# Performance work log

Measured on AMD Instinct MI355X. Metric: run time of the kernel, lower is better.

Reference implementation:

```python
import jax, jax.numpy as jnp
import numpy as np

B, N, C, H = 4, 4096, 1024, 16
D = C // H


def setup_inputs() -> dict:
    key = jax.random.key(0)
    ks = jax.random.split(key, 15)
    s = 0.02
    f = lambda k, shp: jax.random.normal(k, shp, dtype=jnp.float32) * s
    return {
        "x": f(ks[0], (B, N, C)),
        "qkv_w": f(ks[1], (C, 3 * C)),
        "qkv_b": f(ks[2], (3 * C,)),
        "out_w": f(ks[3], (C, C)),
        "out_b": f(ks[4], (C,)),
        # NB: original code dynamically re-creates position_bias as (1, N, H, H)
        # because q/k/v are never transposed to (B,H,N,D); attention runs over heads.
        "pos_bias": f(ks[5], (1, N, H, H)),
        "conv_w": f(ks[6], (C, C)),
        "conv_b": f(ks[7], (C,)),
        "pw_w": f(ks[8], (C, C, 1)),   # Conv1d kernel_size=1: (out, in, k)
        "pw_b": f(ks[9], (C,)),
        "dw_w": f(ks[10], (C, 1, 3)),  # depthwise Conv1d groups=C: (out, in/groups=1, k)
        "dw_b": f(ks[11], (C,)),
        "tok_w": f(ks[12], (C, C)),
        "tok_b": f(ks[13], (C,)),
    }


def reference(x, qkv_w, qkv_b, out_w, out_b, pos_bias,
              conv_w, conv_b, pw_w, pw_b, dw_w, dw_b, tok_w, tok_b):
    b, n, c = x.shape
    h = pos_bias.shape[2]
    d = c // h
    scale = d ** (-0.5)

    # ---- attention branch (faithful to source: heads axis is attended over) ----
    qkv = (x @ qkv_w + qkv_b).reshape(b, n, h, 3 * d)
    q, k, v = jnp.split(qkv, 3, axis=-1)  # each (B, N, H, D)
    scores = jnp.einsum("bnhd,bngd->bnhg", q, k) * scale + pos_bias  # (B, N, H, H)
    attn_w = jax.nn.softmax(scores, axis=-1)
    attn = jnp.einsum("bnhg,bngd->bnhd", attn_w, v).reshape(b, n, c)
    attn = attn @ out_w + out_b

    # ---- convolutional branch ----
    xc = x @ conv_w + conv_b            # (B, N, C)
    xc = xc.transpose(0, 2, 1)          # (B, C, N)
    dn = ("NCH", "OIH", "NCH")
    xc = jax.lax.conv_general_dilated(xc, pw_w, (1,), [(0, 0)],
                                      dimension_numbers=dn) + pw_b[None, :, None]
    xc = jax.lax.conv_general_dilated(xc, dw_w, (1,), [(1, 1)],
                                      dimension_numbers=dn,
                                      feature_group_count=c) + dw_b[None, :, None]
    xc = xc.transpose(0, 2, 1) @ tok_w + tok_b  # (B, N, C)

    return attn + xc
```

## Files before the change

### kernel.cpp

```cpp
#include <hip/hip_runtime.h>
#include <hip/hip_bf16.h>


typedef __attribute__((ext_vector_type(8))) short sh8;
typedef __attribute__((ext_vector_type(4))) float f4;

__device__ __forceinline__ float bf2f(short s) {
  unsigned u = ((unsigned)(unsigned short)s) << 16;
  return __builtin_bit_cast(float, u);
}
__device__ __forceinline__ short f2bf(float f) {
  return __builtin_bit_cast(short, __float2bfloat16(f));
}
__device__ __forceinline__ void g2l16(const void* g, void* l) {
  __builtin_amdgcn_global_load_lds(
      (const __attribute__((address_space(1))) unsigned int*)g,
      (__attribute__((address_space(3))) unsigned int*)l, 16, 0, 0);
}

__global__ __launch_bounds__(256) void cvt_f32_bf16(
    const float* __restrict__ src, short* __restrict__ dst, int n8) {
  int i = blockIdx.x * 256 + threadIdx.x;
  if (i >= n8) return;
  float4 a = ((const float4*)src)[i * 2];
  float4 b = ((const float4*)src)[i * 2 + 1];
  sh8 o;
  o[0] = f2bf(a.x); o[1] = f2bf(a.y); o[2] = f2bf(a.z); o[3] = f2bf(a.w);
  o[4] = f2bf(b.x); o[5] = f2bf(b.y); o[6] = f2bf(b.z); o[7] = f2bf(b.w);
  ((sh8*)dst)[i] = o;
}

__global__ __launch_bounds__(256) void transpose_f32_bf16(
    const float* __restrict__ src, short* __restrict__ dst,
    int N, int ldd, int coff) {
  __shared__ float tile[32][33];
  int kb = blockIdx.y * 32, nb = blockIdx.x * 32;
  int tx = threadIdx.x, ty = threadIdx.y;
#pragma unroll
  for (int j = 0; j < 32; j += 8)
    tile[ty + j][tx] = src[(size_t)(kb + ty + j) * N + nb + tx];
  __syncthreads();
#pragma unroll
  for (int j = 0; j < 32; j += 8)
    dst[(size_t)(nb + ty + j) * ldd + coff + kb + tx] = f2bf(tile[tx][ty + j]);
}

__global__ __launch_bounds__(256) void prep_misc(
    const float* __restrict__ pw_w, const float* __restrict__ conv_b,
    const float* __restrict__ pw_b, const float* __restrict__ out_b,
    const float* __restrict__ tok_b, const float* __restrict__ dw_w,
    const float* __restrict__ dw_b,
    float* __restrict__ b2, float* __restrict__ bcat,
    float* __restrict__ dw0, float* __restrict__ dw1,
    float* __restrict__ dw2, float* __restrict__ dwb) {
  int o = blockIdx.x;
  float part = 0.f;
  for (int i = threadIdx.x; i < 1024; i += 256)
    part += pw_w[(size_t)o * 1024 + i] * conv_b[i];
#pragma unroll
  for (int off = 32; off >= 1; off >>= 1) part += __shfl_down(part, off);
  __shared__ float red[4];
  int wid = threadIdx.x >> 6, lane = threadIdx.x & 63;
  if (lane == 0) red[wid] = part;
  __syncthreads();
  if (threadIdx.x == 0) {
    float s = red[0] + red[1] + red[2] + red[3];
    b2[o] = s + pw_b[o];
    bcat[o] = out_b[o] + tok_b[o];
    dw0[o] = dw_w[o * 3 + 0];
    dw1[o] = dw_w[o * 3 + 1];
    dw2[o] = dw_w[o * 3 + 2];
    dwb[o] = dw_b[o];
  }
}

template <int OUT_BF16>
__global__ __launch_bounds__(256, 2) void gemm128(
    const short* __restrict__ A, const short* __restrict__ Bt,
    void* __restrict__ Cp, const float* __restrict__ bias, int K, int ldc) {
  __shared__ short As[128 * 32];
  __shared__ short Bs[128 * 32];
  const int wid = threadIdx.x >> 6, lane = threadIdx.x & 63;
  const int bm = blockIdx.y, bn = blockIdx.x;
  const int wr = wid >> 1, wc = wid & 1;
  const size_t abase = (size_t)bm * 128 * K;
  const size_t bbase = (size_t)bn * 128 * K;
  const int r16 = lane & 15, ko = (lane >> 4) * 8;

  f4 acc[4][4] = {};

  for (int k0 = 0; k0 < K; k0 += 32) {
    __syncthreads();
#pragma unroll
    for (int c = 0; c < 2; ++c) {
      int ch = c * 256 + wid * 64 + lane;
      int row = ch >> 2, kc = (ch & 3) * 8;
      g2l16(A + abase + (size_t)row * K + k0 + kc, &As[ch * 8]);
      g2l16(Bt + bbase + (size_t)row * K + k0 + kc, &Bs[ch * 8]);
    }
    __syncthreads();
    sh8 af[4], bf[4];
#pragma unroll
    for (int i = 0; i < 4; ++i)
      af[i] = *(const sh8*)&As[(wr * 64 + i * 16 + r16) * 32 + ko];
#pragma unroll
    for (int j = 0; j < 4; ++j)
      bf[j] = *(const sh8*)&Bs[(wc * 64 + j * 16 + r16) * 32 + ko];
#pragma unroll
    for (int i = 0; i < 4; ++i)
#pragma unroll
      for (int j = 0; j < 4; ++j)
        acc[i][j] = __builtin_amdgcn_mfma_f32_16x16x32_bf16(af[i], bf[j],
                                                            acc[i][j], 0, 0, 0);
  }

  const int crow = wr * 64 + (lane >> 4) * 4;
  const int ccol = wc * 64 + r16;
#pragma unroll
  for (int i = 0; i < 4; ++i) {
#pragma unroll
    for (int j = 0; j < 4; ++j) {
      int col = bn * 128 + ccol + j * 16;
      float bv = bias ? bias[col] : 0.f;
#pragma unroll
      for (int r = 0; r < 4; ++r) {
        int row = bm * 128 + crow + i * 16 + r;
        float v = acc[i][j][r] + bv;
        if (OUT_BF16)
          ((short*)Cp)[(size_t)row * ldc + col] = f2bf(v);
        else
          ((float*)Cp)[(size_t)row * ldc + col] = v;
      }
    }
  }
}

template <int OUT_BF16>
__global__ __launch_bounds__(512, 2) void gemm256(
    const short* __restrict__ A, const short* __restrict__ Bt,
    void* __restrict__ Cp, const float* __restrict__ bias,
    int K, int ldc, int nbn) {
  __shared__ short lds[65536];
  const int tid = threadIdx.x;
  const int lane = tid & 63, wid = tid >> 6;
  const int wr = wid >> 2, wc = wid & 3;
  const int r16 = lane & 15;
  const int kidx = ((lane >> 4) ^ ((r16 >> 1) & 3)) << 3;

  const int cpx = gridDim.x >> 3;
  const int swz = (blockIdx.x & 7) * cpx + (blockIdx.x >> 3);
  const int bm = swz / nbn, bn = swz % nbn;

  const short* Ag = A + (size_t)bm * 256 * K;
  const short* Bg = Bt + (size_t)bn * 256 * K;

  int goff0, goff1, loff0, loff1;
  {
    int s0 = tid, row0 = s0 >> 2;
    int kc0 = (s0 & 3) ^ ((row0 >> 1) & 3);
    goff0 = row0 * K + kc0 * 8;
    loff0 = s0 * 8;
    int s1 = 512 + tid, row1 = s1 >> 2;
    int kc1 = (s1 & 3) ^ ((row1 >> 1) & 3);
    goff1 = row1 * K + kc1 * 8;
    loff1 = s1 * 8;
  }

  f4 acc[8][4] = {};
  const int NT = K >> 5;

#define STAGE_FULL(KT, B)                                   \
  do {                                                      \
    short* lb = &lds[(B) * 16384];                          \
    const short* ga = Ag + (KT) * 32;                       \
    const short* gb = Bg + (KT) * 32;                       \
    g2l16(ga + goff0, lb + loff0);                          \
    g2l16(gb + goff0, lb + 8192 + loff0);                   \
    g2l16(ga + goff1, lb + loff1);                          \
    g2l16(gb + goff1, lb + 8192 + loff1);                   \
  } while (0)

  STAGE_FULL(0, 0);
  STAGE_FULL(1, 1);
  asm volatile("s_waitcnt vmcnt(4)" ::: "memory");
  __builtin_amdgcn_sched_barrier(0);
  __builtin_amdgcn_s_barrier();

  for (int t = 0; t < NT; ++t) {
    const short* Ab = &lds[(t & 3) * 16384];
    const short* Bb = Ab + 8192;
    const int kt2 = (t + 2 < NT) ? t + 2 : 0;
    short* lb2 = &lds[((t + 2) & 3) * 16384];
    const short* ga2 = Ag + kt2 * 32;
    const short* gb2 = Bg + kt2 * 32;

    sh8 af[8], bfr[4];

#pragma unroll
    for (int i = 0; i < 4; ++i)
      af[i] = *(const sh8*)&Ab[(wr * 128 + i * 16 + r16) * 32 + kidx];
#pragma unroll
    for (int j = 0; j < 4; ++j)
      bfr[j] = *(const sh8*)&Bb[(wc * 64 + j * 16 + r16) * 32 + kidx];
    g2l16(ga2 + goff0, lb2 + loff0);
    g2l16(gb2 + goff0, lb2 + 8192 + loff0);
    __builtin_amdgcn_sched_barrier(0);
    __builtin_amdgcn_s_barrier();
    asm volatile("s_waitcnt lgkmcnt(0)" ::: "memory");
    __builtin_amdgcn_sched_barrier(0);
    __builtin_amdgcn_s_setprio(1);
#pragma unroll
    for (int i = 0; i < 4; ++i)
#pragma unroll
      for (int j = 0; j < 4; ++j)
        acc[i][j] = __builtin_amdgcn_mfma_f32_16x16x32_bf16(af[i], bfr[j],
                                                            acc[i][j], 0, 0, 0);
    __builtin_amdgcn_s_setprio(0);
    __builtin_amdgcn_sched_barrier(0);
    __builtin_amdgcn_s_barrier();

#pragma unroll
    for (int i = 4; i < 8; ++i)
      af[i] = *(const sh8*)&Ab[(wr * 128 + i * 16 + r16) * 32 + kidx];
    g2l16(ga2 + goff1, lb2 + loff1);
    g2l16(gb2 + goff1, lb2 + 8192 + loff1);
    __builtin_amdgcn_sched_barrier(0);
    __builtin_amdgcn_s_barrier();
    asm volatile("s_waitcnt lgkmcnt(0)" ::: "memory");
    __builtin_amdgcn_sched_barrier(0);
    __builtin_amdgcn_s_setprio(1);
#pragma unroll
    for (int i = 4; i < 8; ++i)
#pragma unroll
      for (int j = 0; j < 4; ++j)
        acc[i][j] = __builtin_amdgcn_mfma_f32_16x16x32_bf16(af[i], bfr[j],
                                                            acc[i][j], 0, 0, 0);
    __builtin_amdgcn_s_setprio(0);
    __builtin_amdgcn_sched_barrier(0);
    asm volatile("s_waitcnt vmcnt(4)" ::: "memory");
    __builtin_amdgcn_s_barrier();
  }
#undef STAGE_FULL

  const int crow0 = bm * 256 + wr * 128 + (lane >> 4) * 4;
  const int ccol0 = bn * 256 + wc * 64 + r16;
  float bv[4];
#pragma unroll
  for (int j = 0; j < 4; ++j) bv[j] = bias ? bias[ccol0 + j * 16] : 0.f;
#pragma unroll
  for (int i = 0; i < 8; ++i) {
#pragma unroll
    for (int r = 0; r < 4; ++r) {
      size_t rowoff = (size_t)(crow0 + i * 16 + r) * ldc + ccol0;
#pragma unroll
      for (int j = 0; j < 4; ++j) {
        float v = acc[i][j][r] + bv[j];
        if (OUT_BF16)
          ((short*)Cp)[rowoff + j * 16] = f2bf(v);
        else
          ((float*)Cp)[rowoff + j * 16] = v;
      }
    }
  }
}

__global__ __launch_bounds__(256) void attn_fused(
    const short* __restrict__ qkv, const float* __restrict__ pos_bias,
    short* __restrict__ xcat) {
  __shared__ short sq[4 * 3072];
  int t0 = blockIdx.x * 4;
  const sh8* gsrc = (const sh8*)(qkv + (size_t)t0 * 3072);
  sh8* ldst = (sh8*)sq;
#pragma unroll
  for (int c = 0; c < 6; ++c) ldst[threadIdx.x + c * 256] = gsrc[threadIdx.x + c * 256];
  __syncthreads();

  int wid = threadIdx.x >> 6, lane = threadIdx.x & 63;
  int t = t0 + wid, n = t & 4095;
  int h = lane >> 2, sub = lane & 3;
  const short* base = sq + wid * 3072 + h * 192;

  float qf[64];
#pragma unroll
  for (int c = 0; c < 8; ++c) {
    sh8 v8 = *(const sh8*)(base + c * 8);
#pragma unroll
    for (int j = 0; j < 8; ++j) qf[c * 8 + j] = bf2f(v8[j]);
  }

  const float* pb = pos_bias + (size_t)n * 256 + h * 16 + sub * 4;
  float p[4];
  float m = -1e30f;
#pragma unroll
  for (int g4 = 0; g4 < 4; ++g4) {
    int g = sub * 4 + g4;
    const short* kk = sq + wid * 3072 + g * 192 + 64;
    float acc = 0.f;
#pragma unroll
    for (int c = 0; c < 8; ++c) {
      sh8 k8 = *(const sh8*)(kk + c * 8);
#pragma unroll
      for (int j = 0; j < 8; ++j) acc += qf[c * 8 + j] * bf2f(k8[j]);
    }
    p[g4] = acc * 0.125f + pb[g4];
    m = fmaxf(m, p[g4]);
  }
  m = fmaxf(m, __shfl_xor(m, 1));
  m = fmaxf(m, __shfl_xor(m, 2));
  float sum = 0.f;
#pragma unroll
  for (int g4 = 0; g4 < 4; ++g4) {
    p[g4] = __expf(p[g4] - m);
    sum += p[g4];
  }
  sum += __shfl_xor(sum, 1);
  sum += __shfl_xor(sum, 2);
  float inv = 1.0f / sum;
#pragma unroll
  for (int g4 = 0; g4 < 4; ++g4) p[g4] *= inv;

  float pall[16];
#pragma unroll
  for (int g = 0; g < 16; ++g)
    pall[g] = __shfl(p[g & 3], (lane & 60) | (g >> 2));

  float o[16] = {};
#pragma unroll
  for (int g = 0; g < 16; ++g) {
    const short* vv = sq + wid * 3072 + g * 192 + 128 + sub * 16;
    sh8 va = *(const sh8*)vv;
    sh8 vb = *(const sh8*)(vv + 8);
#pragma unroll
    for (int j = 0; j < 8; ++j) {
      o[j] += pall[g] * bf2f(va[j]);
      o[8 + j] += pall[g] * bf2f(vb[j]);
    }
  }
  sh8 oa, ob;
#pragma unroll
  for (int j = 0; j < 8; ++j) {
    oa[j] = f2bf(o[j]);
    ob[j] = f2bf(o[8 + j]);
  }
  short* dst = xcat + (size_t)t * 2048 + h * 64 + sub * 16;
  *(sh8*)dst = oa;
  *(sh8*)(dst + 8) = ob;
}

__global__ __launch_bounds__(256) void dwconv(
    const short* __restrict__ xc2, const float* __restrict__ dw0,
    const float* __restrict__ dw1, const float* __restrict__ dw2,
    const float* __restrict__ dwb, short* __restrict__ xcat) {
  int idx = blockIdx.x * 256 + threadIdx.x;
  int t = idx >> 7, c = (idx & 127) * 8;
  int n = t & 4095;
  const short* row = xc2 + (size_t)t * 1024 + c;
  sh8 mid = *(const sh8*)row;
  sh8 lo = {}, hi = {};
  if (n > 0) lo = *(const sh8*)(row - 1024);
  if (n < 4095) hi = *(const sh8*)(row + 1024);
  sh8 out;
#pragma unroll
  for (int j = 0; j < 8; ++j) {
    float v = dw0[c + j] * bf2f(lo[j]) + dw1[c + j] * bf2f(mid[j]) +
              dw2[c + j] * bf2f(hi[j]) + dwb[c + j];
    out[j] = f2bf(v);
  }
  *(sh8*)(xcat + (size_t)t * 2048 + 1024 + c) = out;
}

extern "C" void kernel_launch(void* const* d_in, const int* in_sizes, int n_in,
                              void* d_out, int out_size, void* d_ws,
                              size_t ws_size, hipStream_t stream) {
  const float* x      = (const float*)d_in[0];
  const float* qkv_w  = (const float*)d_in[1];
  const float* qkv_b  = (const float*)d_in[2];
  const float* out_w  = (const float*)d_in[3];
  const float* out_b  = (const float*)d_in[4];
  const float* pos_b  = (const float*)d_in[5];
  const float* conv_w = (const float*)d_in[6];
  const float* conv_b = (const float*)d_in[7];
  const float* pw_w   = (const float*)d_in[8];
  const float* pw_b   = (const float*)d_in[9];
  const float* dw_w   = (const float*)d_in[10];
  const float* dw_b   = (const float*)d_in[11];
  const float* tok_w  = (const float*)d_in[12];
  const float* tok_b  = (const float*)d_in[13];

  const int M = 16384;
  char* ws = (char*)d_ws;
  size_t off = 0;
  auto alloc = [&](size_t bytes) -> void* {
    void* p = ws + off;
    off += (bytes + 255) & ~(size_t)255;
    return p;
  };
  short* xb    = (short*)alloc((size_t)M * 1024 * 2);
  short* qkvwt = (short*)alloc((size_t)3072 * 1024 * 2);
  short* wcatT = (short*)alloc((size_t)1024 * 2048 * 2);
  short* convb = (short*)alloc((size_t)1024 * 1024 * 2);
  short* pwb   = (short*)alloc((size_t)1024 * 1024 * 2);
  short* w2t   = (short*)alloc((size_t)1024 * 1024 * 2);
  short* qkvb  = (short*)alloc((size_t)M * 3072 * 2);
  short* xc2   = (short*)alloc((size_t)M * 1024 * 2);
  short* xcat  = (short*)alloc((size_t)M * 2048 * 2);
  float* b2    = (float*)alloc(1024 * 4);
  float* bcat  = (float*)alloc(1024 * 4);
  float* dw0   = (float*)alloc(1024 * 4);
  float* dw1   = (float*)alloc(1024 * 4);
  float* dw2   = (float*)alloc(1024 * 4);
  float* dwb   = (float*)alloc(1024 * 4);
  (void)ws_size; (void)in_sizes; (void)n_in; (void)out_size;

  cvt_f32_bf16<<<8192, 256, 0, stream>>>(x, xb, M * 1024 / 8);
  cvt_f32_bf16<<<512, 256, 0, stream>>>(conv_w, convb, 1024 * 1024 / 8);
  cvt_f32_bf16<<<512, 256, 0, stream>>>(pw_w, pwb, 1024 * 1024 / 8);
  transpose_f32_bf16<<<dim3(96, 32), dim3(32, 8), 0, stream>>>(qkv_w, qkvwt, 3072, 1024, 0);
  transpose_f32_bf16<<<dim3(32, 32), dim3(32, 8), 0, stream>>>(out_w, wcatT, 1024, 2048, 0);
  transpose_f32_bf16<<<dim3(32, 32), dim3(32, 8), 0, stream>>>(tok_w, wcatT, 1024, 2048, 1024);
  prep_misc<<<1024, 256, 0, stream>>>(pw_w, conv_b, pw_b, out_b, tok_b, dw_w,
                                      dw_b, b2, bcat, dw0, dw1, dw2, dwb);
  gemm128<1><<<dim3(8, 8), 256, 0, stream>>>(pwb, convb, w2t, nullptr, 1024, 1024);

  gemm256<1><<<768, 512, 0, stream>>>(xb, qkvwt, qkvb, qkv_b, 1024, 3072, 12);
  gemm256<1><<<256, 512, 0, stream>>>(xb, w2t, xc2, b2, 1024, 1024, 4);

  attn_fused<<<4096, 256, 0, stream>>>(qkvb, pos_b, xcat);
  dwconv<<<8192, 256, 0, stream>>>(xc2, dw0, dw1, dw2, dwb, xcat);

  gemm256<0><<<256, 512, 0, stream>>>(xcat, wcatT, d_out, bcat, 2048, 1024, 4);
}
```

Measured before the change: 343.2 us.

## Switch main GEMMs to 256x128 tiles with 4 waves and triple-buffered LDS

```diff
diff --git a/kernel.cpp b/kernel.cpp
--- a/kernel.cpp
+++ b/kernel.cpp
@@ -136,14 +136,14 @@
 }
 
 template <int OUT_BF16>
-__global__ __launch_bounds__(512, 2) void gemm256(
+__global__ __launch_bounds__(256, 2) void gemmMain(
     const short* __restrict__ A, const short* __restrict__ Bt,
     void* __restrict__ Cp, const float* __restrict__ bias,
     int K, int ldc, int nbn) {
-  __shared__ short lds[65536];
+  __shared__ short lds[36864];
   const int tid = threadIdx.x;
   const int lane = tid & 63, wid = tid >> 6;
-  const int wr = wid >> 2, wc = wid & 3;
+  const int wr = wid >> 1, wc = wid & 1;
   const int r16 = lane & 15;
   const int kidx = ((lane >> 4) ^ ((r16 >> 1) & 3)) << 3;
 
@@ -152,45 +152,51 @@
   const int bm = swz / nbn, bn = swz % nbn;
 
   const short* Ag = A + (size_t)bm * 256 * K;
-  const short* Bg = Bt + (size_t)bn * 256 * K;
-
-  int goff0, goff1, loff0, loff1;
-  {
-    int s0 = tid, row0 = s0 >> 2;
-    int kc0 = (s0 & 3) ^ ((row0 >> 1) & 3);
-    goff0 = row0 * K + kc0 * 8;
-    loff0 = s0 * 8;
-    int s1 = 512 + tid, row1 = s1 >> 2;
-    int kc1 = (s1 & 3) ^ ((row1 >> 1) & 3);
-    goff1 = row1 * K + kc1 * 8;
-    loff1 = s1 * 8;
+  const short* Bg = Bt + (size_t)bn * 128 * K;
+
+  int gA[4], lA[4], gB[2], lB[2];
+#pragma unroll
+  for (int r = 0; r < 4; ++r) {
+    int ch = r * 256 + tid, row = ch >> 2;
+    int kc = (ch & 3) ^ ((row >> 1) & 3);
+    gA[r] = row * K + kc * 8;
+    lA[r] = ch * 8;
+  }
+#pragma unroll
+  for (int r = 0; r < 2; ++r) {
+    int ch = r * 256 + tid, row = ch >> 2;
+    int kc = (ch & 3) ^ ((row >> 1) & 3);
+    gB[r] = row * K + kc * 8;
+    lB[r] = 8192 + ch * 8;
   }
 
   f4 acc[8][4] = {};
   const int NT = K >> 5;
 
-#define STAGE_FULL(KT, B)                                   \
+#define STAGE6(KT, BUF)                                     \
   do {                                                      \
-    short* lb = &lds[(B) * 16384];                          \
+    short* lb = &lds[(BUF) * 12288];                        \
     const short* ga = Ag + (KT) * 32;                       \
     const short* gb = Bg + (KT) * 32;                       \
-    g2l16(ga + goff0, lb + loff0);                          \
-    g2l16(gb + goff0, lb + 8192 + loff0);                   \
-    g2l16(ga + goff1, lb + loff1);                          \
-    g2l16(gb + goff1, lb + 8192 + loff1);                   \
+    g2l16(ga + gA[0], lb + lA[0]);                          \
+    g2l16(ga + gA[1], lb + lA[1]);                          \
+    g2l16(ga + gA[2], lb + lA[2]);                          \
+    g2l16(ga + gA[3], lb + lA[3]);                          \
+    g2l16(gb + gB[0], lb + lB[0]);                          \
+    g2l16(gb + gB[1], lb + lB[1]);                          \
   } while (0)
 
-  STAGE_FULL(0, 0);
-  STAGE_FULL(1, 1);
-  asm volatile("s_waitcnt vmcnt(4)" ::: "memory");
+  STAGE6(0, 0);
+  STAGE6(1, 1);
+  asm volatile("s_waitcnt vmcnt(6)" ::: "memory");
   __builtin_amdgcn_sched_barrier(0);
   __builtin_amdgcn_s_barrier();
 
   for (int t = 0; t < NT; ++t) {
-    const short* Ab = &lds[(t & 3) * 16384];
+    const short* Ab = &lds[(t % 3) * 12288];
     const short* Bb = Ab + 8192;
     const int kt2 = (t + 2 < NT) ? t + 2 : 0;
-    short* lb2 = &lds[((t + 2) & 3) * 16384];
+    short* lb2 = &lds[((t + 2) % 3) * 12288];
     const short* ga2 = Ag + kt2 * 32;
     const short* gb2 = Bg + kt2 * 32;
 
@@ -202,8 +208,9 @@
 #pragma unroll
     for (int j = 0; j < 4; ++j)
       bfr[j] = *(const sh8*)&Bb[(wc * 64 + j * 16 + r16) * 32 + kidx];
-    g2l16(ga2 + goff0, lb2 + loff0);
-    g2l16(gb2 + goff0, lb2 + 8192 + loff0);
+    g2l16(ga2 + gA[0], lb2 + lA[0]);
+    g2l16(ga2 + gA[1], lb2 + lA[1]);
+    g2l16(gb2 + gB[0], lb2 + lB[0]);
     __builtin_amdgcn_sched_barrier(0);
     __builtin_amdgcn_s_barrier();
     asm volatile("s_waitcnt lgkmcnt(0)" ::: "memory");
@@ -222,8 +229,9 @@
 #pragma unroll
     for (int i = 4; i < 8; ++i)
       af[i] = *(const sh8*)&Ab[(wr * 128 + i * 16 + r16) * 32 + kidx];
-    g2l16(ga2 + goff1, lb2 + loff1);
-    g2l16(gb2 + goff1, lb2 + 8192 + loff1);
+    g2l16(ga2 + gA[2], lb2 + lA[2]);
+    g2l16(ga2 + gA[3], lb2 + lA[3]);
+    g2l16(gb2 + gB[1], lb2 + lB[1]);
     __builtin_amdgcn_sched_barrier(0);
     __builtin_amdgcn_s_barrier();
     asm volatile("s_waitcnt lgkmcnt(0)" ::: "memory");
@@ -237,13 +245,13 @@
                                                             acc[i][j], 0, 0, 0);
     __builtin_amdgcn_s_setprio(0);
     __builtin_amdgcn_sched_barrier(0);
-    asm volatile("s_waitcnt vmcnt(4)" ::: "memory");
+    asm volatile("s_waitcnt vmcnt(6)" ::: "memory");
     __builtin_amdgcn_s_barrier();
   }
-#undef STAGE_FULL
+#undef STAGE6
 
   const int crow0 = bm * 256 + wr * 128 + (lane >> 4) * 4;
-  const int ccol0 = bn * 256 + wc * 64 + r16;
+  const int ccol0 = bn * 128 + wc * 64 + r16;
   float bv[4];
 #pragma unroll
   for (int j = 0; j < 4; ++j) bv[j] = bias ? bias[ccol0 + j * 16] : 0.f;
@@ -422,11 +430,11 @@
                                       dw_b, b2, bcat, dw0, dw1, dw2, dwb);
   gemm128<1><<<dim3(8, 8), 256, 0, stream>>>(pwb, convb, w2t, nullptr, 1024, 1024);
 
-  gemm256<1><<<768, 512, 0, stream>>>(xb, qkvwt, qkvb, qkv_b, 1024, 3072, 12);
-  gemm256<1><<<256, 512, 0, stream>>>(xb, w2t, xc2, b2, 1024, 1024, 4);
+  gemmMain<1><<<1536, 256, 0, stream>>>(xb, qkvwt, qkvb, qkv_b, 1024, 3072, 24);
+  gemmMain<1><<<512, 256, 0, stream>>>(xb, w2t, xc2, b2, 1024, 1024, 8);
 
   attn_fused<<<4096, 256, 0, stream>>>(qkvb, pos_b, xcat);
   dwconv<<<8192, 256, 0, stream>>>(xc2, dw0, dw1, dw2, dwb, xcat);
 
-  gemm256<0><<<256, 512, 0, stream>>>(xcat, wcatT, d_out, bcat, 2048, 1024, 4);
-}
+  gemmMain<0><<<512, 256, 0, stream>>>(xcat, wcatT, d_out, bcat, 2048, 1024, 8);
+}
```

After: 344.8 us. About the same (+0.5%).

## Merge QKV and conv projection GEMMs into one wide GEMM and simplify pipeline

Applied to the files above, without the earlier changes.

```diff
diff --git a/kernel.cpp b/kernel.cpp
--- a/kernel.cpp
+++ b/kernel.cpp
@@ -47,31 +47,34 @@
 
 __global__ __launch_bounds__(256) void prep_misc(
     const float* __restrict__ pw_w, const float* __restrict__ conv_b,
-    const float* __restrict__ pw_b, const float* __restrict__ out_b,
-    const float* __restrict__ tok_b, const float* __restrict__ dw_w,
-    const float* __restrict__ dw_b,
-    float* __restrict__ b2, float* __restrict__ bcat,
+    const float* __restrict__ pw_b, const float* __restrict__ qkv_b,
+    const float* __restrict__ out_b, const float* __restrict__ tok_b,
+    const float* __restrict__ dw_w, const float* __restrict__ dw_b,
+    float* __restrict__ bias4, float* __restrict__ bcat,
     float* __restrict__ dw0, float* __restrict__ dw1,
     float* __restrict__ dw2, float* __restrict__ dwb) {
   int o = blockIdx.x;
-  float part = 0.f;
-  for (int i = threadIdx.x; i < 1024; i += 256)
-    part += pw_w[(size_t)o * 1024 + i] * conv_b[i];
-#pragma unroll
-  for (int off = 32; off >= 1; off >>= 1) part += __shfl_down(part, off);
-  __shared__ float red[4];
-  int wid = threadIdx.x >> 6, lane = threadIdx.x & 63;
-  if (lane == 0) red[wid] = part;
-  __syncthreads();
-  if (threadIdx.x == 0) {
-    float s = red[0] + red[1] + red[2] + red[3];
-    b2[o] = s + pw_b[o];
-    bcat[o] = out_b[o] + tok_b[o];
-    dw0[o] = dw_w[o * 3 + 0];
-    dw1[o] = dw_w[o * 3 + 1];
-    dw2[o] = dw_w[o * 3 + 2];
-    dwb[o] = dw_b[o];
-  }
+  if (o < 1024) {
+    float part = 0.f;
+    for (int i = threadIdx.x; i < 1024; i += 256)
+      part += pw_w[(size_t)o * 1024 + i] * conv_b[i];
+#pragma unroll
+    for (int off = 32; off >= 1; off >>= 1) part += __shfl_down(part, off);
+    __shared__ float red[4];
+    int wid = threadIdx.x >> 6, lane = threadIdx.x & 63;
+    if (lane == 0) red[wid] = part;
+    __syncthreads();
+    if (threadIdx.x == 0) {
+      float s = red[0] + red[1] + red[2] + red[3];
+      bias4[3072 + o] = s + pw_b[o];
+      bcat[o] = out_b[o] + tok_b[o];
+      dw0[o] = dw_w[o * 3 + 0];
+      dw1[o] = dw_w[o * 3 + 1];
+      dw2[o] = dw_w[o * 3 + 2];
+      dwb[o] = dw_b[o];
+    }
+  }
+  if (threadIdx.x == 0) bias4[o] = qkv_b[o];
 }
 
 template <int OUT_BF16>
@@ -185,52 +188,28 @@
   asm volatile("s_waitcnt vmcnt(4)" ::: "memory");
   __builtin_amdgcn_sched_barrier(0);
   __builtin_amdgcn_s_barrier();
+  __builtin_amdgcn_sched_barrier(0);
 
   for (int t = 0; t < NT; ++t) {
     const short* Ab = &lds[(t & 3) * 16384];
     const short* Bb = Ab + 8192;
     const int kt2 = (t + 2 < NT) ? t + 2 : 0;
-    short* lb2 = &lds[((t + 2) & 3) * 16384];
-    const short* ga2 = Ag + kt2 * 32;
-    const short* gb2 = Bg + kt2 * 32;
+    STAGE_FULL(kt2, (t + 2) & 3);
 
     sh8 af[8], bfr[4];
-
 #pragma unroll
     for (int i = 0; i < 4; ++i)
       af[i] = *(const sh8*)&Ab[(wr * 128 + i * 16 + r16) * 32 + kidx];
 #pragma unroll
     for (int j = 0; j < 4; ++j)
       bfr[j] = *(const sh8*)&Bb[(wc * 64 + j * 16 + r16) * 32 + kidx];
-    g2l16(ga2 + goff0, lb2 + loff0);
-    g2l16(gb2 + goff0, lb2 + 8192 + loff0);
-    __builtin_amdgcn_sched_barrier(0);
-    __builtin_amdgcn_s_barrier();
-    asm volatile("s_waitcnt lgkmcnt(0)" ::: "memory");
-    __builtin_amdgcn_sched_barrier(0);
-    __builtin_amdgcn_s_setprio(1);
-#pragma unroll
-    for (int i = 0; i < 4; ++i)
-#pragma unroll
-      for (int j = 0; j < 4; ++j)
-        acc[i][j] = __builtin_amdgcn_mfma_f32_16x16x32_bf16(af[i], bfr[j],
-                                                            acc[i][j], 0, 0, 0);
-    __builtin_amdgcn_s_setprio(0);
-    __builtin_amdgcn_sched_barrier(0);
-    __builtin_amdgcn_s_barrier();
-
 #pragma unroll
     for (int i = 4; i < 8; ++i)
       af[i] = *(const sh8*)&Ab[(wr * 128 + i * 16 + r16) * 32 + kidx];
-    g2l16(ga2 + goff1, lb2 + loff1);
-    g2l16(gb2 + goff1, lb2 + 8192 + loff1);
-    __builtin_amdgcn_sched_barrier(0);
-    __builtin_amdgcn_s_barrier();
-    asm volatile("s_waitcnt lgkmcnt(0)" ::: "memory");
-    __builtin_amdgcn_sched_barrier(0);
+
     __builtin_amdgcn_s_setprio(1);
 #pragma unroll
-    for (int i = 4; i < 8; ++i)
+    for (int i = 0; i < 8; ++i)
 #pragma unroll
       for (int j = 0; j < 4; ++j)
         acc[i][j] = __builtin_amdgcn_mfma_f32_16x16x32_bf16(af[i], bfr[j],
@@ -238,7 +217,9 @@
     __builtin_amdgcn_s_setprio(0);
     __builtin_amdgcn_sched_barrier(0);
     asm volatile("s_waitcnt vmcnt(4)" ::: "memory");
+    __builtin_amdgcn_sched_barrier(0);
     __builtin_amdgcn_s_barrier();
+    __builtin_amdgcn_sched_barrier(0);
   }
 #undef STAGE_FULL
 
@@ -265,14 +246,18 @@
 }
 
 __global__ __launch_bounds__(256) void attn_fused(
-    const short* __restrict__ qkv, const float* __restrict__ pos_bias,
+    const short* __restrict__ qkvx, const float* __restrict__ pos_bias,
     short* __restrict__ xcat) {
   __shared__ short sq[4 * 3072];
   int t0 = blockIdx.x * 4;
-  const sh8* gsrc = (const sh8*)(qkv + (size_t)t0 * 3072);
-  sh8* ldst = (sh8*)sq;
-#pragma unroll
-  for (int c = 0; c < 6; ++c) ldst[threadIdx.x + c * 256] = gsrc[threadIdx.x + c * 256];
+#pragma unroll
+  for (int c = 0; c < 6; ++c) {
+    int g = c * 256 + threadIdx.x;
+    int tok = (g * 683) >> 18;
+    int off = g - tok * 384;
+    ((sh8*)sq)[tok * 384 + off] =
+        *(const sh8*)(qkvx + (size_t)(t0 + tok) * 4096 + off * 8);
+  }
   __syncthreads();
 
   int wid = threadIdx.x >> 6, lane = threadIdx.x & 63;
@@ -348,17 +333,17 @@
 }
 
 __global__ __launch_bounds__(256) void dwconv(
-    const short* __restrict__ xc2, const float* __restrict__ dw0,
+    const short* __restrict__ qkvx, const float* __restrict__ dw0,
     const float* __restrict__ dw1, const float* __restrict__ dw2,
     const float* __restrict__ dwb, short* __restrict__ xcat) {
   int idx = blockIdx.x * 256 + threadIdx.x;
   int t = idx >> 7, c = (idx & 127) * 8;
   int n = t & 4095;
-  const short* row = xc2 + (size_t)t * 1024 + c;
+  const short* row = qkvx + (size_t)t * 4096 + 3072 + c;
   sh8 mid = *(const sh8*)row;
   sh8 lo = {}, hi = {};
-  if (n > 0) lo = *(const sh8*)(row - 1024);
-  if (n < 4095) hi = *(const sh8*)(row + 1024);
+  if (n > 0) lo = *(const sh8*)(row - 4096);
+  if (n < 4095) hi = *(const sh8*)(row + 4096);
   sh8 out;
 #pragma unroll
   for (int j = 0; j < 8; ++j) {
@@ -396,15 +381,13 @@
     return p;
   };
   short* xb    = (short*)alloc((size_t)M * 1024 * 2);
-  short* qkvwt = (short*)alloc((size_t)3072 * 1024 * 2);
+  short* wbig  = (short*)alloc((size_t)4096 * 1024 * 2);
   short* wcatT = (short*)alloc((size_t)1024 * 2048 * 2);
   short* convb = (short*)alloc((size_t)1024 * 1024 * 2);
   short* pwb   = (short*)alloc((size_t)1024 * 1024 * 2);
-  short* w2t   = (short*)alloc((size_t)1024 * 1024 * 2);
-  short* qkvb  = (short*)alloc((size_t)M * 3072 * 2);
-  short* xc2   = (short*)alloc((size_t)M * 1024 * 2);
+  short* qkvx  = (short*)alloc((size_t)M * 4096 * 2);
   short* xcat  = (short*)alloc((size_t)M * 2048 * 2);
-  float* b2    = (float*)alloc(1024 * 4);
+  float* bias4 = (float*)alloc(4096 * 4);
   float* bcat  = (float*)alloc(1024 * 4);
   float* dw0   = (float*)alloc(1024 * 4);
   float* dw1   = (float*)alloc(1024 * 4);
@@ -415,18 +398,18 @@
   cvt_f32_bf16<<<8192, 256, 0, stream>>>(x, xb, M * 1024 / 8);
   cvt_f32_bf16<<<512, 256, 0, stream>>>(conv_w, convb, 1024 * 1024 / 8);
   cvt_f32_bf16<<<512, 256, 0, stream>>>(pw_w, pwb, 1024 * 1024 / 8);
-  transpose_f32_bf16<<<dim3(96, 32), dim3(32, 8), 0, stream>>>(qkv_w, qkvwt, 3072, 1024, 0);
+  transpose_f32_bf16<<<dim3(96, 32), dim3(32, 8), 0, stream>>>(qkv_w, wbig, 3072, 1024, 0);
   transpose_f32_bf16<<<dim3(32, 32), dim3(32, 8), 0, stream>>>(out_w, wcatT, 1024, 2048, 0);
   transpose_f32_bf16<<<dim3(32, 32), dim3(32, 8), 0, stream>>>(tok_w, wcatT, 1024, 2048, 1024);
-  prep_misc<<<1024, 256, 0, stream>>>(pw_w, conv_b, pw_b, out_b, tok_b, dw_w,
-                                      dw_b, b2, bcat, dw0, dw1, dw2, dwb);
-  gemm128<1><<<dim3(8, 8), 256, 0, stream>>>(pwb, convb, w2t, nullptr, 1024, 1024);
-
-  gemm256<1><<<768, 512, 0, stream>>>(xb, qkvwt, qkvb, qkv_b, 1024, 3072, 12);
-  gemm256<1><<<256, 512, 0, stream>>>(xb, w2t, xc2, b2, 1024, 1024, 4);
-
-  attn_fused<<<4096, 256, 0, stream>>>(qkvb, pos_b, xcat);
-  dwconv<<<8192, 256, 0, stream>>>(xc2, dw0, dw1, dw2, dwb, xcat);
+  prep_misc<<<3072, 256, 0, stream>>>(pw_w, conv_b, pw_b, qkv_b, out_b, tok_b,
+                                      dw_w, dw_b, bias4, bcat, dw0, dw1, dw2, dwb);
+  gemm128<1><<<dim3(8, 8), 256, 0, stream>>>(pwb, convb, wbig + (size_t)3072 * 1024,
+                                             nullptr, 1024, 1024);
+
+  gemm256<1><<<1024, 512, 0, stream>>>(xb, wbig, qkvx, bias4, 1024, 4096, 16);
+
+  attn_fused<<<4096, 256, 0, stream>>>(qkvx, pos_b, xcat);
+  dwconv<<<8192, 256, 0, stream>>>(qkvx, dw0, dw1, dw2, dwb, xcat);
 
   gemm256<0><<<256, 512, 0, stream>>>(xcat, wcatT, d_out, bcat, 2048, 1024, 4);
 }
```

After: 338.4 us. No clear change (-1.4%).
